# Optimization experiments

Measured on AMD Instinct MI355X. Metric: run time of the kernel, lower is better.

Reference implementation:

```python
import jax, jax.numpy as jnp
import numpy as np

# ---- config (from init_kwargs) ----
BASE_SIZE = 16
RATIOS = np.array([0.5, 1.0, 2.0])
N_LAYERS = 3
SCALES = 2.0 ** np.arange(N_LAYERS)
STRIDE = 16
PRE_NMS_TOPN = 2000
POST_NMS_TOPN = 300
MIN_THRESHOLD = 16.0
NMS_THRESH = 0.7
IMG_W = 1024
IMG_H = 1024
B, H, W = 16, 64, 64
A = len(RATIOS) * len(SCALES)  # 9


def _whctrs(a):
    w = a[2] - a[0] + 1.0
    h = a[3] - a[1] + 1.0
    return w, h, a[0] + 0.5 * (w - 1.0), a[1] + 0.5 * (h - 1.0)


def _mkanchors(ws, hs, cx, cy):
    return np.stack([cx - 0.5 * (ws - 1.0), cy - 0.5 * (hs - 1.0),
                     cx + 0.5 * (ws - 1.0), cy + 0.5 * (hs - 1.0)], axis=1)


def _generate_anchors():
    base = np.array([0.0, 0.0, BASE_SIZE - 1.0, BASE_SIZE - 1.0])
    w, h, cx, cy = _whctrs(base)
    size = w * h
    ws = np.round(np.sqrt(size / RATIOS))
    hs = np.round(ws * RATIOS)
    ratio_anchors = _mkanchors(ws, hs, np.full_like(ws, cx), np.full_like(ws, cy))
    out = []
    for ra in ratio_anchors:
        rw, rh, rcx, rcy = _whctrs(ra)
        out.append(_mkanchors(rw * SCALES, rh * SCALES,
                              np.full_like(SCALES, rcx), np.full_like(SCALES, rcy)))
    return np.concatenate(out, axis=0)  # (A, 4)


def _all_anchors(height, width):
    anchors = _generate_anchors()  # (A, 4)
    sx = np.arange(width) * STRIDE
    sy = np.arange(height) * STRIDE
    sx, sy = np.meshgrid(sx, sy)  # (H, W) row-major over y -> matches permute(0,2,3,1)
    shifts = np.stack([sx.ravel(), sy.ravel(), sx.ravel(), sy.ravel()], axis=1)  # (K, 4)
    return (anchors[None, :, :] + shifts[:, None, :]).reshape(-1, 4).astype(np.float32)  # (K*A, 4)


def _decode(deltas, anchors):
    # bbox_reg_to_coord: standard bbox_transform_inv
    aw = anchors[:, 2] - anchors[:, 0] + 1.0
    ah = anchors[:, 3] - anchors[:, 1] + 1.0
    acx = anchors[:, 0] + 0.5 * aw
    acy = anchors[:, 1] + 0.5 * ah
    cx = deltas[..., 0] * aw + acx
    cy = deltas[..., 1] * ah + acy
    pw = jnp.exp(deltas[..., 2]) * aw
    ph = jnp.exp(deltas[..., 3]) * ah
    return jnp.stack([cx - 0.5 * pw, cy - 0.5 * ph,
                      cx + 0.5 * pw, cy + 0.5 * ph], axis=-1)


def _nms_single(boxes, scores):
    # boxes: (N, 4) sorted by descending score
    N = boxes.shape[0]
    x1, y1, x2, y2 = boxes[:, 0], boxes[:, 1], boxes[:, 2], boxes[:, 3]
    areas = (x2 - x1 + 1.0) * (y2 - y1 + 1.0)
    iw = jnp.maximum(0.0, jnp.minimum(x2[:, None], x2[None, :]) - jnp.maximum(x1[:, None], x1[None, :]) + 1.0)
    ih = jnp.maximum(0.0, jnp.minimum(y2[:, None], y2[None, :]) - jnp.maximum(y1[:, None], y1[None, :]) + 1.0)
    inter = iw * ih
    iou = inter / (areas[:, None] + areas[None, :] - inter)  # (N, N)
    idx = jnp.arange(N)

    def body(sup, i):  # greedy sequential NMS
        keep_i = ~sup[i]
        sup = sup | (keep_i & (iou[i] > NMS_THRESH) & (idx > i))
        return sup, keep_i

    _, keep = jax.lax.scan(body, jnp.zeros(N, dtype=bool), idx)
    # kept boxes first, preserving score order; fixed-size output padded with zeros
    prio = jnp.where(keep, idx, idx + N)
    order = jnp.argsort(prio)[:POST_NMS_TOPN]
    valid = keep[order]
    out_boxes = jnp.where(valid[:, None], boxes[order], 0.0)
    out_scores = jnp.where(valid, scores[order], 0.0)
    return out_boxes, out_scores


def reference(labels_pred, bbox_reg):
    b, _, h, w = labels_pred.shape
    anchors = jnp.asarray(_all_anchors(h, w))  # (K*A, 4)
    scores = labels_pred.transpose(0, 2, 3, 1).reshape(b, -1, 2)[..., 1]  # (B, K*A)
    deltas = bbox_reg.transpose(0, 2, 3, 1).reshape(b, -1, 4)  # (B, K*A, 4)
    boxes = _decode(deltas, anchors)
    boxes = jnp.stack([
        jnp.clip(boxes[..., 0], 0.0, IMG_W - 1.0),
        jnp.clip(boxes[..., 1], 0.0, IMG_H - 1.0),
        jnp.clip(boxes[..., 2], 0.0, IMG_W - 1.0),
        jnp.clip(boxes[..., 3], 0.0, IMG_H - 1.0)], axis=-1)
    keep = ((boxes[..., 2] - boxes[..., 0] + 1.0 >= MIN_THRESHOLD)
            & (boxes[..., 3] - boxes[..., 1] + 1.0 >= MIN_THRESHOLD))
    masked = jnp.where(keep, scores, -jnp.inf)
    top_scores, top_idx = jax.lax.top_k(masked, PRE_NMS_TOPN)  # (B, pre)
    top_boxes = jnp.take_along_axis(boxes, top_idx[..., None], axis=1)  # (B, pre, 4)
    return jax.vmap(_nms_single)(top_boxes, top_scores)


def setup_inputs() -> dict:
    key = jax.random.key(0)
    k1, k2 = jax.random.split(key)
    labels_pred = jax.random.normal(k1, (B, 2 * A, H, W), dtype=jnp.float32)
    bbox_reg = jax.random.normal(k2, (B, 4 * A, H, W), dtype=jnp.float32) * 0.2
    return {"labels_pred": labels_pred, "bbox_reg": bbox_reg}
```

## Files before the change

kernel.cpp:

```cpp
#include <hip/hip_runtime.h>
#include <stdint.h>

#pragma clang fp contract(off)

typedef unsigned long long ull;

#define NB 16
#define NA 9
#define HW 4096
#define NANCH (NA*HW)
#define TOTAL (NB*NANCH)
#define TOPN 2000
#define PADN 2048
#define SELPAD 3072
#define OUTN 300
#define HBITS 13
#define HBINS (1 << HBITS)
#define MNMS 384
#define MSTRIPS (MNMS/64)
#define GDN 8

#define MIDC 0x1.666667p-1

__constant__ float c_ax1[9] = {-3.5f,-15.f,-38.f,  0.f, -8.f,-24.f,  2.5f, -3.f,-14.f};
__constant__ float c_ay1[9] = { 2.f,  -4.f,-16.f,  0.f, -8.f,-24.f, -3.f,-14.f,-36.f};
__constant__ float c_ax2[9] = {18.5f, 30.f, 53.f, 15.f, 23.f, 39.f, 12.5f, 18.f, 29.f};
__constant__ float c_ay2[9] = {13.f,  19.f, 31.f, 15.f, 23.f, 39.f, 18.f,  29.f, 51.f};

__device__ __forceinline__ void decode_box(int a, int x, int y,
    float d0, float d1, float d2, float d3,
    float& x1, float& y1, float& x2, float& y2) {
  float ax1 = c_ax1[a] + 16.f * (float)x;
  float ay1 = c_ay1[a] + 16.f * (float)y;
  float ax2 = c_ax2[a] + 16.f * (float)x;
  float ay2 = c_ay2[a] + 16.f * (float)y;
  float aw  = ax2 - ax1 + 1.f;
  float ah  = ay2 - ay1 + 1.f;
  float acx = ax1 + 0.5f * aw;
  float acy = ay1 + 0.5f * ah;
  float cx = d0 * aw + acx;
  float cy = d1 * ah + acy;
  float pw = expf(d2) * aw;
  float ph = expf(d3) * ah;
  x1 = cx - 0.5f * pw;
  y1 = cy - 0.5f * ph;
  x2 = cx + 0.5f * pw;
  y2 = cy + 0.5f * ph;
  x1 = fminf(fmaxf(x1, 0.f), 1023.f);
  y1 = fminf(fmaxf(y1, 0.f), 1023.f);
  x2 = fminf(fmaxf(x2, 0.f), 1023.f);
  y2 = fminf(fmaxf(y2, 0.f), 1023.f);
}

__device__ __forceinline__ uint32_t f2ord(float f) {
  uint32_t u = __float_as_uint(f);
  return (u & 0x80000000u) ? ~u : (u | 0x80000000u);
}
__device__ __forceinline__ float ord2f(uint32_t u) {
  return (u & 0x80000000u) ? __uint_as_float(u ^ 0x80000000u) : __uint_as_float(~u);
}

__global__ void k_score(const float* __restrict__ labels, const float* __restrict__ bbox,
                        uint32_t* __restrict__ keys) {
  int t = blockIdx.x * 256 + threadIdx.x;
  if (t >= TOTAL) return;
  int pos = t & (HW - 1);
  int ba  = t >> 12;
  int a = ba % 9, b = ba / 9;
  float score = labels[((b * 18 + 2 * a + 1) << 12) + pos];
  const float* dp = bbox + ((b * 36 + 4 * a) << 12) + pos;
  float d0 = dp[0], d1 = dp[4096], d2 = dp[8192], d3 = dp[12288];
  int y = pos >> 6, x = pos & 63;
  float x1, y1, x2, y2;
  decode_box(a, x, y, d0, d1, d2, d3, x1, y1, x2, y2);
  bool keep = (x2 - x1 + 1.f >= 16.f) && (y2 - y1 + 1.f >= 16.f);
  float s = keep ? score : -INFINITY;
  keys[t] = f2ord(s);
}

__global__ __launch_bounds__(1024) void k_batch(const uint32_t* __restrict__ keys,
                                                ull* __restrict__ selKeys,
                                                uint32_t* __restrict__ counters) {
  int b = blockIdx.x, tid = threadIdx.x;
  int wave = tid >> 6, lane = tid & 63;
  __shared__ uint32_t hist[HBINS];
  __shared__ uint32_t wtot[16];
  __shared__ uint32_t sh_T, sh_cnt;
  const uint32_t* kb = keys + b * NANCH;
  const uint4* kb4 = (const uint4*)kb;
#pragma unroll
  for (int k = 0; k < HBINS / 1024; ++k) hist[k * 1024 + tid] = 0u;
  if (tid == 0) { sh_T = 0u; sh_cnt = 0u; }
  __syncthreads();
  for (int i4 = tid; i4 < NANCH / 4; i4 += 1024) {
    uint4 v = kb4[i4];
    if (v.x & 0x80000000u) atomicAdd(&hist[v.x >> (32 - HBITS)], 1u);
    if (v.y & 0x80000000u) atomicAdd(&hist[v.y >> (32 - HBITS)], 1u);
    if (v.z & 0x80000000u) atomicAdd(&hist[v.z >> (32 - HBITS)], 1u);
    if (v.w & 0x80000000u) atomicAdd(&hist[v.w >> (32 - HBITS)], 1u);
  }
  __syncthreads();
  uint32_t c[8], suf[8];
#pragma unroll
  for (int k = 0; k < 8; ++k) c[k] = hist[tid * 8 + k];
  suf[7] = c[7];
#pragma unroll
  for (int k = 6; k >= 0; --k) suf[k] = c[k] + suf[k + 1];
  uint32_t total = suf[0];
  uint32_t wsuf = total;
#pragma unroll
  for (int off = 1; off < 64; off <<= 1) {
    uint32_t v = __shfl_down(wsuf, off);
    if (lane + off < 64) wsuf += v;
  }
  if (lane == 0) wtot[wave] = wsuf;
  __syncthreads();
  uint32_t wab = 0;
  for (int w = wave + 1; w < 16; ++w) wab += wtot[w];
  uint32_t ssum = wsuf + wab;
  uint32_t above_t = ssum - total;
  if (above_t < TOPN && ssum >= TOPN) {
    uint32_t T = (uint32_t)(tid * 8);
#pragma unroll
    for (int k = 7; k >= 0; --k) {
      uint32_t ab = above_t + ((k < 7) ? suf[k + 1] : 0u);
      if (ab < TOPN && ab + c[k] >= TOPN) T = (uint32_t)(tid * 8 + k);
    }
    sh_T = T;
  }
  __syncthreads();
  uint32_t T = sh_T;
  for (int i4 = tid; i4 < NANCH / 4; i4 += 1024) {
    uint4 v = kb4[i4];
    uint32_t vv[4] = { v.x, v.y, v.z, v.w };
#pragma unroll
    for (int cc = 0; cc < 4; ++cc) {
      uint32_t u = vv[cc];
      if ((u >> (32 - HBITS)) >= T) {
        uint32_t slot = atomicAdd(&sh_cnt, 1u);
        if (slot < SELPAD) {
          int i = i4 * 4 + cc;
          uint32_t canon = (uint32_t)((i & 4095) * 9 + (i >> 12));
          selKeys[b * SELPAD + slot] = (((ull)(~u)) << 32) | canon;
        }
      }
    }
  }
  __syncthreads();
  if (tid == 0) counters[b] = (sh_cnt < SELPAD) ? sh_cnt : SELPAD;
}

__global__ __launch_bounds__(256) void k_rank(const ull* __restrict__ selKeys,
                        const uint32_t* __restrict__ counters, const float* __restrict__ bbox,
                        float4* __restrict__ boxes, float* __restrict__ areas,
                        float* __restrict__ selScore) {
  int b = blockIdx.y;
  int i = blockIdx.x * 256 + threadIdx.x;
  int tid = threadIdx.x;
  uint32_t n = counters[b];
  const ull* sk = selKeys + b * SELPAD;
  ull ki = (i < (int)n) ? sk[i] : ~0ull;
  int rank = 0;
  __shared__ ull chunk[256];
  for (uint32_t base = 0; base < n; base += 256) {
    uint32_t j = base + (uint32_t)tid;
    chunk[tid] = (j < n) ? sk[j] : ~0ull;
    __syncthreads();
    int lim = (int)(n - base < 256u ? n - base : 256u);
    for (int t2 = 0; t2 < lim; ++t2) rank += (chunk[t2] < ki) ? 1 : 0;
    __syncthreads();
  }
  if (i < (int)n && rank < TOPN) {
    uint32_t idx = (uint32_t)ki;
    selScore[b * TOPN + rank] = ord2f(~((uint32_t)(ki >> 32)));
    int pos = (int)idx / 9, a = (int)idx - 9 * pos;
    int y = pos >> 6, x = pos & 63;
    const float* dp = bbox + ((b * 36 + 4 * a) << 12) + pos;
    float d0 = dp[0], d1 = dp[4096], d2 = dp[8192], d3 = dp[12288];
    float x1, y1, x2, y2;
    decode_box(a, x, y, d0, d1, d2, d3, x1, y1, x2, y2);
    boxes[b * PADN + rank] = make_float4(x1, y1, x2, y2);
    areas[b * PADN + rank] = (x2 - x1 + 1.f) * (y2 - y1 + 1.f);
  }
}

__global__ __launch_bounds__(1024) void k_nms(const float4* __restrict__ boxes,
                                              const float* __restrict__ areas,
                                              const float* __restrict__ selScore,
                                              float* __restrict__ out) {
  int b = blockIdx.x, tid = threadIdx.x;
  int wv = tid >> 6, lane = tid & 63;
  __shared__ float4 sbox[MNMS];
  __shared__ float  sar[MNMS];
  __shared__ ull    mrowU[MNMS][8];
  __shared__ int    kidx[OUTN];
  __shared__ int    sh_cnt;
  if (tid < MNMS) {
    sbox[tid] = boxes[b * PADN + tid];
    sar[tid]  = areas[b * PADN + tid];
  }
  __syncthreads();
  const double MD = MIDC;
#pragma unroll
  for (int s = 0; s < MSTRIPS; ++s) {
    int j = (s << 6) + lane;
    float4 bj = sbox[j];
    float  ja = sar[j];
    int rmax = (s + 1) << 6; if (rmax > MNMS) rmax = MNMS;
    for (int i = wv; i < rmax; i += 16) {
      float4 bi = sbox[i];
      float  ia = sar[i];
      float iw = fminf(bi.z, bj.z) - fmaxf(bi.x, bj.x) + 1.f; iw = fmaxf(iw, 0.f);
      float ih = fminf(bi.w, bj.w) - fmaxf(bi.y, bj.y) + 1.f; ih = fmaxf(ih, 0.f);
      float inter = iw * ih;
      float uu = (ia + ja) - inter;
      bool sup = (j > i) && ((double)inter >= MD * (double)uu);
      ull mb = __ballot(sup);
      if (lane == 0) mrowU[i][s] = mb;
    }
  }
  __syncthreads();
  if (tid < 64) {
    int l8 = lane & 7;
    ull supw = 0ull;
    int cnt = 0;
    ull pf[GDN];
#pragma unroll
    for (int ph = 0; ph < GDN; ++ph) pf[ph] = mrowU[ph][l8];
    for (int base = 0; base < MNMS && cnt < OUTN; base += GDN) {
#pragma unroll
      for (int ph = 0; ph < GDN; ++ph) {
        int i = base + ph;
        ull bal = __ballot(((supw >> (i & 63)) & 1ull) != 0ull);
        if (!((bal >> (i >> 6)) & 1ull)) {
          ull mm = (l8 >= (i >> 6) && l8 < MSTRIPS) ? pf[ph] : 0ull;
          supw |= mm;
          if (lane == 0 && cnt < OUTN) kidx[cnt] = i;
          cnt++;
        }
        int nx = i + GDN; if (nx > MNMS - 1) nx = MNMS - 1;
        pf[ph] = mrowU[nx][l8];
      }
    }
    for (int i = MNMS; i < TOPN && cnt < OUTN; ++i) {
      float4 bi = boxes[b * PADN + i];
      float ia = areas[b * PADN + i];
      bool sup = false;
      for (int cb = 0; cb < cnt; cb += 64) {
        int k = cb + lane;
        if (k < cnt) {
          int kj = kidx[k];
          float4 bk = boxes[b * PADN + kj];
          float ka = areas[b * PADN + kj];
          float iw = fminf(bi.z, bk.z) - fmaxf(bi.x, bk.x) + 1.f; iw = fmaxf(iw, 0.f);
          float ih = fminf(bi.w, bk.w) - fmaxf(bi.y, bk.y) + 1.f; ih = fmaxf(ih, 0.f);
          float inter = iw * ih;
          float uu = (ia + ka) - inter;
          sup = sup || ((double)inter >= MD * (double)uu);
        }
      }
      if (!__any(sup)) {
        if (lane == 0) kidx[cnt] = i;
        cnt++;
      }
    }
    if (lane == 0) sh_cnt = (cnt < OUTN) ? cnt : OUTN;
  }
  __syncthreads();
  int c = sh_cnt;
  float4* ob = (float4*)out;
  for (int s2 = tid; s2 < OUTN; s2 += 1024) {
    float4 bx = make_float4(0.f, 0.f, 0.f, 0.f);
    float sc = 0.f;
    if (s2 < c) {
      int i = kidx[s2];
      bx = boxes[b * PADN + i];
      sc = selScore[b * TOPN + i];
    }
    ob[b * OUTN + s2] = bx;
    out[NB * OUTN * 4 + b * OUTN + s2] = sc;
  }
}

extern "C" void kernel_launch(void* const* d_in, const int* in_sizes, int n_in,
                              void* d_out, int out_size, void* d_ws, size_t ws_size,
                              hipStream_t stream) {
  const float* labels = (const float*)d_in[0];
  const float* bbox   = (const float*)d_in[1];
  char* ws = (char*)d_ws;
  uint32_t* keys    = (uint32_t*)(ws + 0);
  ull* selKeys      = (ull*)(ws + 2359296);
  float* selScore   = (float*)(ws + 2752512);
  float* areas      = (float*)(ws + 2880512);
  float4* boxes     = (float4*)(ws + 3011584);
  uint32_t* counters= (uint32_t*)(ws + 3535872);
  float* out = (float*)d_out;

  hipLaunchKernelGGL(k_score, dim3((TOTAL + 255) / 256), dim3(256), 0, stream, labels, bbox, keys);
  hipLaunchKernelGGL(k_batch, dim3(NB), dim3(1024), 0, stream, keys, selKeys, counters);
  hipLaunchKernelGGL(k_rank,  dim3(SELPAD / 256, NB), dim3(256), 0, stream, selKeys, counters, bbox, boxes, areas, selScore);
  hipLaunchKernelGGL(k_nms,   dim3(NB), dim3(1024), 0, stream, boxes, areas, selScore, out);
}
```

Baseline: 99.99 us.

## Split NMS into parallel mask kernel and single-wave scan kernel

The fused per-batch NMS kernel, which ran on 16 blocks, is split in two. A mask kernel computes the 384x384 suppression bitmask over a grid of 12x16 blocks and writes it to global workspace. A 64-thread scan kernel then reads the mask rows from global memory with a deeper prefetch of 16 rows. This spreads the IoU work across many more CUs, at the cost of an extra launch, a global-memory round trip for the mask, and a scan that waits on global loads instead of LDS.

```diff
diff --git a/kernel.cpp b/kernel.cpp
--- a/kernel.cpp
+++ b/kernel.cpp
@@ -18,7 +18,8 @@
 #define HBINS (1 << HBITS)
 #define MNMS 384
 #define MSTRIPS (MNMS/64)
-#define GDN 8
+#define MPITCH 8
+#define GD2 16
 
 #define MIDC 0x1.666667p-1
 
@@ -184,92 +185,107 @@
   }
 }
 
-__global__ __launch_bounds__(1024) void k_nms(const float4* __restrict__ boxes,
+__global__ __launch_bounds__(256) void k_mask(const float4* __restrict__ boxes,
                                               const float* __restrict__ areas,
-                                              const float* __restrict__ selScore,
-                                              float* __restrict__ out) {
-  int b = blockIdx.x, tid = threadIdx.x;
-  int wv = tid >> 6, lane = tid & 63;
-  __shared__ float4 sbox[MNMS];
-  __shared__ float  sar[MNMS];
-  __shared__ ull    mrowU[MNMS][8];
-  __shared__ int    kidx[OUTN];
-  __shared__ int    sh_cnt;
-  if (tid < MNMS) {
-    sbox[tid] = boxes[b * PADN + tid];
-    sar[tid]  = areas[b * PADN + tid];
+                                              ull* __restrict__ gmask) {
+  int rb = blockIdx.x, b = blockIdx.y;
+  int tid = threadIdx.x, wv = tid >> 6, lane = tid & 63;
+  int rbase = rb * 32;
+  int smin = rbase >> 6;
+  __shared__ float4 sRow[32];
+  __shared__ float  sAr[32];
+  if (tid < 32) {
+    sRow[tid] = boxes[b * PADN + rbase + tid];
+    sAr[tid]  = areas[b * PADN + rbase + tid];
+  }
+  float4 bj[MSTRIPS];
+  float  ja[MSTRIPS];
+#pragma unroll
+  for (int s = 0; s < MSTRIPS; ++s) {
+    if (s >= smin) {
+      bj[s] = boxes[b * PADN + (s << 6) + lane];
+      ja[s] = areas[b * PADN + (s << 6) + lane];
+    }
   }
   __syncthreads();
   const double MD = MIDC;
-#pragma unroll
-  for (int s = 0; s < MSTRIPS; ++s) {
-    int j = (s << 6) + lane;
-    float4 bj = sbox[j];
-    float  ja = sar[j];
-    int rmax = (s + 1) << 6; if (rmax > MNMS) rmax = MNMS;
-    for (int i = wv; i < rmax; i += 16) {
-      float4 bi = sbox[i];
-      float  ia = sar[i];
-      float iw = fminf(bi.z, bj.z) - fmaxf(bi.x, bj.x) + 1.f; iw = fmaxf(iw, 0.f);
-      float ih = fminf(bi.w, bj.w) - fmaxf(bi.y, bj.y) + 1.f; ih = fmaxf(ih, 0.f);
+  for (int r = wv; r < 32; r += 4) {
+    int i = rbase + r;
+    float4 bi = sRow[r];
+    float  ia = sAr[r];
+#pragma unroll
+    for (int s = 0; s < MSTRIPS; ++s) {
+      if (s < smin) continue;
+      int j = (s << 6) + lane;
+      float iw = fminf(bi.z, bj[s].z) - fmaxf(bi.x, bj[s].x) + 1.f; iw = fmaxf(iw, 0.f);
+      float ih = fminf(bi.w, bj[s].w) - fmaxf(bi.y, bj[s].y) + 1.f; ih = fmaxf(ih, 0.f);
       float inter = iw * ih;
-      float uu = (ia + ja) - inter;
+      float uu = (ia + ja[s]) - inter;
       bool sup = (j > i) && ((double)inter >= MD * (double)uu);
       ull mb = __ballot(sup);
-      if (lane == 0) mrowU[i][s] = mb;
-    }
-  }
-  __syncthreads();
-  if (tid < 64) {
-    int l8 = lane & 7;
-    ull supw = 0ull;
-    int cnt = 0;
-    ull pf[GDN];
-#pragma unroll
-    for (int ph = 0; ph < GDN; ++ph) pf[ph] = mrowU[ph][l8];
-    for (int base = 0; base < MNMS && cnt < OUTN; base += GDN) {
-#pragma unroll
-      for (int ph = 0; ph < GDN; ++ph) {
-        int i = base + ph;
-        ull bal = __ballot(((supw >> (i & 63)) & 1ull) != 0ull);
-        if (!((bal >> (i >> 6)) & 1ull)) {
-          ull mm = (l8 >= (i >> 6) && l8 < MSTRIPS) ? pf[ph] : 0ull;
-          supw |= mm;
-          if (lane == 0 && cnt < OUTN) kidx[cnt] = i;
-          cnt++;
-        }
-        int nx = i + GDN; if (nx > MNMS - 1) nx = MNMS - 1;
-        pf[ph] = mrowU[nx][l8];
-      }
-    }
-    for (int i = MNMS; i < TOPN && cnt < OUTN; ++i) {
-      float4 bi = boxes[b * PADN + i];
-      float ia = areas[b * PADN + i];
-      bool sup = false;
-      for (int cb = 0; cb < cnt; cb += 64) {
-        int k = cb + lane;
-        if (k < cnt) {
-          int kj = kidx[k];
-          float4 bk = boxes[b * PADN + kj];
-          float ka = areas[b * PADN + kj];
-          float iw = fminf(bi.z, bk.z) - fmaxf(bi.x, bk.x) + 1.f; iw = fmaxf(iw, 0.f);
-          float ih = fminf(bi.w, bk.w) - fmaxf(bi.y, bk.y) + 1.f; ih = fmaxf(ih, 0.f);
-          float inter = iw * ih;
-          float uu = (ia + ka) - inter;
-          sup = sup || ((double)inter >= MD * (double)uu);
-        }
-      }
-      if (!__any(sup)) {
-        if (lane == 0) kidx[cnt] = i;
+      if (lane == 0) gmask[((size_t)b * MNMS + i) * MPITCH + s] = mb;
+    }
+  }
+}
+
+__global__ __launch_bounds__(64) void k_scan(const ull* __restrict__ gmask,
+                                             const float4* __restrict__ boxes,
+                                             const float* __restrict__ areas,
+                                             const float* __restrict__ selScore,
+                                             float* __restrict__ out) {
+  int b = blockIdx.x, lane = threadIdx.x;
+  const ull* mb = gmask + (size_t)b * MNMS * MPITCH;
+  int l8 = lane & 7;
+  __shared__ int kidx[OUTN];
+  __shared__ int sh_cnt;
+  const double MD = MIDC;
+  ull supw = 0ull;
+  int cnt = 0;
+  ull pf[GD2];
+#pragma unroll
+  for (int ph = 0; ph < GD2; ++ph) pf[ph] = mb[ph * MPITCH + l8];
+  for (int base = 0; base < MNMS && cnt < OUTN; base += GD2) {
+#pragma unroll
+    for (int ph = 0; ph < GD2; ++ph) {
+      int i = base + ph;
+      ull bal = __ballot(((supw >> (i & 63)) & 1ull) != 0ull);
+      if (!((bal >> (i >> 6)) & 1ull)) {
+        ull mm = (l8 >= (i >> 6) && l8 < MSTRIPS) ? pf[ph] : 0ull;
+        supw |= mm;
+        if (lane == 0 && cnt < OUTN) kidx[cnt] = i;
         cnt++;
       }
-    }
-    if (lane == 0) sh_cnt = (cnt < OUTN) ? cnt : OUTN;
-  }
+      int nx = i + GD2; if (nx > MNMS - 1) nx = MNMS - 1;
+      pf[ph] = mb[nx * MPITCH + l8];
+    }
+  }
+  for (int i = MNMS; i < TOPN && cnt < OUTN; ++i) {
+    float4 bi = boxes[b * PADN + i];
+    float ia = areas[b * PADN + i];
+    bool sup = false;
+    for (int cb = 0; cb < cnt; cb += 64) {
+      int k = cb + lane;
+      if (k < cnt) {
+        int kj = kidx[k];
+        float4 bk = boxes[b * PADN + kj];
+        float ka = areas[b * PADN + kj];
+        float iw = fminf(bi.z, bk.z) - fmaxf(bi.x, bk.x) + 1.f; iw = fmaxf(iw, 0.f);
+        float ih = fminf(bi.w, bk.w) - fmaxf(bi.y, bk.y) + 1.f; ih = fmaxf(ih, 0.f);
+        float inter = iw * ih;
+        float uu = (ia + ka) - inter;
+        sup = sup || ((double)inter >= MD * (double)uu);
+      }
+    }
+    if (!__any(sup)) {
+      if (lane == 0) kidx[cnt] = i;
+      cnt++;
+    }
+  }
+  if (lane == 0) sh_cnt = (cnt < OUTN) ? cnt : OUTN;
   __syncthreads();
   int c = sh_cnt;
   float4* ob = (float4*)out;
-  for (int s2 = tid; s2 < OUTN; s2 += 1024) {
+  for (int s2 = lane; s2 < OUTN; s2 += 64) {
     float4 bx = make_float4(0.f, 0.f, 0.f, 0.f);
     float sc = 0.f;
     if (s2 < c) {
@@ -294,10 +310,12 @@
   float* areas      = (float*)(ws + 2880512);
   float4* boxes     = (float4*)(ws + 3011584);
   uint32_t* counters= (uint32_t*)(ws + 3535872);
+  ull* gmask        = (ull*)(ws + 3535936);
   float* out = (float*)d_out;
 
   hipLaunchKernelGGL(k_score, dim3((TOTAL + 255) / 256), dim3(256), 0, stream, labels, bbox, keys);
   hipLaunchKernelGGL(k_batch, dim3(NB), dim3(1024), 0, stream, keys, selKeys, counters);
   hipLaunchKernelGGL(k_rank,  dim3(SELPAD / 256, NB), dim3(256), 0, stream, selKeys, counters, bbox, boxes, areas, selScore);
-  hipLaunchKernelGGL(k_nms,   dim3(NB), dim3(1024), 0, stream, boxes, areas, selScore, out);
-}
+  hipLaunchKernelGGL(k_mask,  dim3(MNMS / 32, NB), dim3(256), 0, stream, boxes, areas, gmask);
+  hipLaunchKernelGGL(k_scan,  dim3(NB), dim3(64), 0, stream, gmask, boxes, areas, selScore, out);
+}
```

Measured after the change: 90.42 us. -9.6%, faster.
